# Performance work log

Hardware: AMD Instinct MI355X
Metric: run time of the kernel (lower is better)

The kernel has to match this reference:

```python
import jax, jax.numpy as jnp
import numpy as np

TOPK = 2  # n_activated
HID, INTER, E, SHARED_INTER = 2048, 1408, 14, 2816


def setup_inputs() -> dict:
    key = jax.random.key(0)
    ks = jax.random.split(key, 11)
    s = 0.02  # weight init scale
    return {
        "x": jax.random.normal(ks[0], (4, 512, HID), jnp.float32),
        "gate_w": jax.random.normal(ks[1], (E, HID), jnp.float32) * s,
        "cls_w": jax.random.normal(ks[2], (E, HID), jnp.float32) * s,
        "extra_scale": jax.random.normal(ks[3], (E,), jnp.float32) * 0.1,
        "extra_bias": jax.random.normal(ks[4], (E,), jnp.float32) * 0.01,
        "wg": jax.random.normal(ks[5], (E, INTER, HID), jnp.float32) * s,
        "wu": jax.random.normal(ks[6], (E, INTER, HID), jnp.float32) * s,
        "wd": jax.random.normal(ks[7], (E, HID, INTER), jnp.float32) * s,
        "sg": jax.random.normal(ks[8], (SHARED_INTER, HID), jnp.float32) * s,
        "su": jax.random.normal(ks[9], (SHARED_INTER, HID), jnp.float32) * s,
        "sd": jax.random.normal(ks[10], (HID, SHARED_INTER), jnp.float32) * s,
    }


def reference(x, gate_w, cls_w, extra_scale, extra_bias, wg, wu, wd, sg, su, sd):
    shape = x.shape
    d = shape[-1]
    xf = x.reshape(-1, d)                      # [T, d]
    T = xf.shape[0]
    n_exp = gate_w.shape[0]

    # Router: scores = softmax(|classifier(x) * silu(gate(x))|)
    logits = (xf @ cls_w.T) * jax.nn.silu(xf @ gate_w.T)        # [T, E]
    scores = jax.nn.softmax(jnp.abs(logits).astype(jnp.float32), axis=-1)
    biased = scores + extra_bias[None, :]
    _, idx = jax.lax.top_k(biased, TOPK)                         # [T, K]
    orig = 1.0 + scores * extra_scale[None, :]
    w = jnp.take_along_axis(orig, idx, axis=1).astype(x.dtype)   # [T, K]

    # Dense combine weights: zero for unrouted (token, expert) pairs.
    combine = jnp.zeros((T, n_exp), x.dtype).at[
        jnp.arange(T)[:, None], idx].add(w)                      # [T, E]

    # Routed experts (SwiGLU MLPs), computed densely then masked-combined.
    g = jax.nn.silu(jnp.einsum('td,efd->etf', xf, wg))           # [E, T, f]
    u = jnp.einsum('td,efd->etf', xf, wu)
    o = jnp.einsum('etf,edf->etd', g * u, wd)                    # [E, T, d]
    y = jnp.einsum('etd,te->td', o, combine)                     # [T, d]

    # Shared expert on all tokens.
    z = (jax.nn.silu(xf @ sg.T) * (xf @ su.T)) @ sd.T            # [T, d]

    return (y + z).reshape(shape)
```

## Files before the change

kernel.cpp:

```cpp
#include <hip/hip_runtime.h>

#define HID 2048
#define INTER 1408
#define NEXP 14
#define SINTER 2816
#define TTOK 2048
#define BM 384
#define BK 64

#define GLU_SH 264
#define GLU_RT 308
#define DWN_SH 96
#define DWN_RT 224

typedef short bf16x8 __attribute__((ext_vector_type(8)));
typedef float f32x4 __attribute__((ext_vector_type(4)));
typedef unsigned short u16x8 __attribute__((ext_vector_type(8)));

__device__ __forceinline__ unsigned short f2bf(float f) {
    __bf16 b = (__bf16)f;
    return __builtin_bit_cast(unsigned short, b);
}
__device__ __forceinline__ float bf2f(unsigned short u) {
    unsigned v = (unsigned)u << 16;
    return __builtin_bit_cast(float, v);
}
__device__ __forceinline__ unsigned swz(unsigned b) { return b ^ (((b >> 7) & 7u) << 4); }

__device__ __forceinline__ void gload16(const void* g, void* l) {
    __builtin_amdgcn_global_load_lds((__attribute__((address_space(1))) void*)g,
                                     (__attribute__((address_space(3))) void*)l, 16, 0, 0);
}
__device__ __forceinline__ void bsync() {
    __builtin_amdgcn_sched_barrier(0);
    __builtin_amdgcn_s_barrier();
    __builtin_amdgcn_sched_barrier(0);
}
#define WAIT_LGKM0 asm volatile("s_waitcnt lgkmcnt(0)" ::: "memory")

__global__ void k_zero(int* cnt) {
    if ((int)threadIdx.x < NEXP) cnt[threadIdx.x] = 0;
}

__global__ __launch_bounds__(256, 4) void k_router(
    const float* __restrict__ x,
    const float* __restrict__ gate_w, const float* __restrict__ cls_w,
    const float* __restrict__ escale, const float* __restrict__ ebias,
    int* __restrict__ cnt, int* __restrict__ etok, float* __restrict__ ew,
    unsigned short* __restrict__ xb) {
    const int lane = threadIdx.x & 63;
    const int tok = blockIdx.x * 4 + (threadIdx.x >> 6);
    const float* xr = x + (size_t)tok * HID + lane * 4;
    float4 xv[8];
#pragma unroll
    for (int i = 0; i < 8; i++) xv[i] = *(const float4*)(xr + i * 256);
    unsigned short* xbr = xb + (size_t)tok * HID + lane * 4;
#pragma unroll
    for (int i = 0; i < 8; i++) {
        ushort4 v;
        v.x = f2bf(xv[i].x); v.y = f2bf(xv[i].y);
        v.z = f2bf(xv[i].z); v.w = f2bf(xv[i].w);
        *(ushort4*)(xbr + i * 256) = v;
    }

    float sc[NEXP];
    float mx = 0.f;
#pragma unroll
    for (int e = 0; e < NEXP; e++) {
        const float* cw = cls_w + (size_t)e * HID + lane * 4;
        const float* gw = gate_w + (size_t)e * HID + lane * 4;
        float pc = 0.f, pg = 0.f;
        {
            float4 cv[8];
#pragma unroll
            for (int i = 0; i < 8; i++) cv[i] = *(const float4*)(cw + i * 256);
#pragma unroll
            for (int i = 0; i < 8; i++) {
                pc = fmaf(xv[i].x, cv[i].x, pc);
                pc = fmaf(xv[i].y, cv[i].y, pc);
                pc = fmaf(xv[i].z, cv[i].z, pc);
                pc = fmaf(xv[i].w, cv[i].w, pc);
            }
        }
        {
            float4 gv[8];
#pragma unroll
            for (int i = 0; i < 8; i++) gv[i] = *(const float4*)(gw + i * 256);
#pragma unroll
            for (int i = 0; i < 8; i++) {
                pg = fmaf(xv[i].x, gv[i].x, pg);
                pg = fmaf(xv[i].y, gv[i].y, pg);
                pg = fmaf(xv[i].z, gv[i].z, pg);
                pg = fmaf(xv[i].w, gv[i].w, pg);
            }
        }
#pragma unroll
        for (int o = 32; o >= 1; o >>= 1) {
            pc += __shfl_xor(pc, o);
            pg += __shfl_xor(pg, o);
        }
        float lg = pc * (pg / (1.f + __expf(-pg)));
        sc[e] = fabsf(lg);
        mx = fmaxf(mx, sc[e]);
    }
    float s = 0.f;
#pragma unroll
    for (int e = 0; e < NEXP; e++) { sc[e] = __expf(sc[e] - mx); s += sc[e]; }
    float inv = 1.f / s;
    int i1 = -1, i2 = -1;
    float b1 = -1e30f, b2 = -1e30f, v1 = 0.f, v2 = 0.f;
#pragma unroll
    for (int e = 0; e < NEXP; e++) {
        float sv = sc[e] * inv;
        float b = sv + ebias[e];
        if (b > b1) { b2 = b1; i2 = i1; v2 = v1; b1 = b; i1 = e; v1 = sv; }
        else if (b > b2) { b2 = b; i2 = e; v2 = sv; }
    }
    if (lane == 0) {
        float w1 = 1.f + v1 * escale[i1];
        float w2 = 1.f + v2 * escale[i2];
        int p1 = atomicAdd(&cnt[i1], 1);
        etok[i1 * TTOK + p1] = tok * 2;     ew[i1 * TTOK + p1] = w1;
        int p2 = atomicAdd(&cnt[i2], 1);
        etok[i2 * TTOK + p2] = tok * 2 + 1; ew[i2 * TTOK + p2] = w2;
    }
}

__global__ void k_offsets(const int* __restrict__ cnt, int* __restrict__ offs) {
    if (threadIdx.x == 0) {
        int a = 0;
        for (int e = 0; e < NEXP; e++) { offs[e] = a; a += cnt[e]; }
    }
}

__global__ __launch_bounds__(1024, 4) void k_glu16(
    const unsigned short* __restrict__ xb,
    const float* __restrict__ wg, const float* __restrict__ wu,
    const float* __restrict__ sg, const float* __restrict__ su,
    unsigned short* __restrict__ abuf, unsigned short* __restrict__ hbuf,
    const int* __restrict__ cnt, const int* __restrict__ offs,
    const int* __restrict__ etok) {
    __shared__ alignas(16) unsigned short sA[2][BM * BK];
    __shared__ alignas(16) unsigned short sBg[64 * BK];
    __shared__ alignas(16) unsigned short sBu[64 * BK];

    const int bx = blockIdx.x, t = threadIdx.x;
    const int lane = t & 63, w = t >> 6;
    const int wm = w >> 1, wn = w & 1;
    const int fr = lane & 15, fo = lane >> 4;

    const bool routed = bx >= GLU_SH;
    int n0, m_start, m_stop, obase, Ntot;
    const float *Bg, *Bu;
    unsigned short* outp;
    const int* etk = nullptr;
    if (routed) {
        int rx = bx - GLU_SH;
        int e = rx / 22; n0 = (rx % 22) * 64;
        int M = cnt[e];
        if (M <= 0) return;
        m_start = 0; m_stop = M; obase = offs[e]; Ntot = INTER;
        Bg = wg + ((size_t)e * INTER + n0) * HID;
        Bu = wu + ((size_t)e * INTER + n0) * HID;
        outp = abuf; etk = etok + e * TTOK;
    } else {
        n0 = (bx / 6) * 64;
        m_start = (bx % 6) * BM; m_stop = min(TTOK, m_start + BM);
        obase = 0; Ntot = SINTER;
        Bg = sg + (size_t)n0 * HID;
        Bu = su + (size_t)n0 * HID;
        outp = hbuf;
    }

    const int brow = t >> 4, bc4 = (t & 15) * 4;
    const float* srcG = Bg + (size_t)brow * HID + bc4;
    const float* srcU = Bu + (size_t)brow * HID + bc4;
    const unsigned wBo = swz((unsigned)(brow * 128 + bc4 * 2));

    unsigned aoff[3][2], boff[2][2];
#pragma unroll
    for (int mi = 0; mi < 3; mi++)
#pragma unroll
        for (int ks = 0; ks < 2; ks++)
            aoff[mi][ks] = swz((unsigned)((wm * 48 + mi * 16 + fr) * 128 + ks * 64 + fo * 16));
#pragma unroll
    for (int nj = 0; nj < 2; nj++)
#pragma unroll
        for (int ks = 0; ks < 2; ks++)
            boff[nj][ks] = swz((unsigned)((wn * 32 + nj * 16 + fr) * 128 + ks * 64 + fo * 16));

    const int arow_off = lane >> 3;
    const int achunk = (lane & 7) ^ arow_off;

    for (int m0 = m_start; m0 < m_stop; m0 += BM) {
        const int rv = min(m_stop - m0, BM);
        const unsigned short* srcA[3];
#pragma unroll
        for (int j = 0; j < 3; j++) {
            int r = (w * 3 + j) * 8 + arow_off;
            int rr = r < rv ? r : rv - 1;
            int tok = routed ? (etk[m0 + rr] >> 1) : (m0 + rr);
            srcA[j] = xb + (size_t)tok * HID + achunk * 8;
        }

        f32x4 ag[3][2], au[3][2];
#pragma unroll
        for (int mi = 0; mi < 3; mi++)
#pragma unroll
            for (int nj = 0; nj < 2; nj++) { ag[mi][nj] = {0.f,0.f,0.f,0.f}; au[mi][nj] = {0.f,0.f,0.f,0.f}; }

#pragma unroll
        for (int j = 0; j < 3; j++)
            gload16(srcA[j], (char*)sA + (w * 3 + j) * 1024);
        float4 gC = *(const float4*)(srcG);
        float4 uC = *(const float4*)(srcU);
        float4 gN, uN;

        for (int kk = 0; kk < HID / BK; ++kk) {
            const int cur = kk & 1;
            bsync();
            if (kk + 1 < HID / BK) {
                const int k0n = (kk + 1) * BK;
#pragma unroll
                for (int j = 0; j < 3; j++)
                    gload16(srcA[j] + k0n, (char*)sA + (cur ^ 1) * (BM * BK * 2) + (w * 3 + j) * 1024);
                gN = *(const float4*)(srcG + k0n);
                uN = *(const float4*)(srcU + k0n);
            }
            __builtin_amdgcn_sched_barrier(0);
            {
                ushort4 vg, vu;
                vg.x = f2bf(gC.x); vg.y = f2bf(gC.y); vg.z = f2bf(gC.z); vg.w = f2bf(gC.w);
                vu.x = f2bf(uC.x); vu.y = f2bf(uC.y); vu.z = f2bf(uC.z); vu.w = f2bf(uC.w);
                *(ushort4*)((char*)sBg + wBo) = vg;
                *(ushort4*)((char*)sBu + wBo) = vu;
            }
            WAIT_LGKM0;
            bsync();
            const char* sAc = (const char*)sA + cur * (BM * BK * 2);
#pragma unroll
            for (int ks = 0; ks < 2; ++ks) {
                bf16x8 af[3], gf[2], uf[2];
#pragma unroll
                for (int mi = 0; mi < 3; mi++) af[mi] = *(const bf16x8*)(sAc + aoff[mi][ks]);
#pragma unroll
                for (int nj = 0; nj < 2; nj++) {
                    gf[nj] = *(const bf16x8*)((const char*)sBg + boff[nj][ks]);
                    uf[nj] = *(const bf16x8*)((const char*)sBu + boff[nj][ks]);
                }
#pragma unroll
                for (int mi = 0; mi < 3; mi++)
#pragma unroll
                    for (int nj = 0; nj < 2; nj++) {
                        ag[mi][nj] = __builtin_amdgcn_mfma_f32_16x16x32_bf16(af[mi], gf[nj], ag[mi][nj], 0, 0, 0);
                        au[mi][nj] = __builtin_amdgcn_mfma_f32_16x16x32_bf16(af[mi], uf[nj], au[mi][nj], 0, 0, 0);
                    }
            }
            gC = gN; uC = uN;
        }

        char* sH = (char*)sA;
#pragma unroll
        for (int mi = 0; mi < 3; mi++)
#pragma unroll
            for (int jj = 0; jj < 4; jj++) {
                int r = wm * 48 + mi * 16 + fo * 4 + jj;
#pragma unroll
                for (int nj = 0; nj < 2; nj++) {
                    int c = wn * 32 + nj * 16 + fr;
                    float g = ag[mi][nj][jj];
                    float u = au[mi][nj][jj];
                    float h = (g / (1.f + __expf(-g))) * u;
                    *(unsigned short*)(sH + swz((unsigned)(r * 128 + c * 2))) = f2bf(h);
                }
            }
        WAIT_LGKM0;
        bsync();
#pragma unroll
        for (int q = 0; q < 3; q++) {
            int idx = q * 1024 + t;
            int r = idx >> 3, c = idx & 7;
            if (r < rv) {
                uint4 v = *(const uint4*)(sH + swz((unsigned)(r * 128 + c * 16)));
                *(uint4*)(outp + (size_t)(obase + m0 + r) * Ntot + n0 + c * 8) = v;
            }
        }
        bsync();
    }
}

__global__ __launch_bounds__(1024, 4) void k_down16(
    const unsigned short* __restrict__ abuf, const unsigned short* __restrict__ hbuf,
    const float* __restrict__ wd, const float* __restrict__ sd,
    unsigned short* __restrict__ slots,
    const int* __restrict__ cnt, const int* __restrict__ offs,
    const int* __restrict__ etok, const float* __restrict__ ew) {
    __shared__ alignas(16) unsigned short sA[2][BM * BK];
    __shared__ alignas(16) unsigned short sB[128 * BK];

    const int bx = blockIdx.x, t = threadIdx.x;
    const int lane = t & 63, w = t >> 6;
    const int wm = w >> 1, wn = w & 1;
    const int fr = lane & 15, fo = lane >> 4;

    const bool routed = bx >= DWN_SH;
    int n0, m_start, m_stop, K, KT;
    const float* W;
    const unsigned short* Abuf;
    size_t arow0 = 0;
    const int* etk = nullptr; const float* ewe = nullptr;
    if (routed) {
        int rx = bx - DWN_SH;
        int e = rx / 16; n0 = (rx % 16) * 128;
        int M = cnt[e];
        if (M <= 0) return;
        m_start = 0; m_stop = M;
        K = INTER; KT = INTER / BK;
        W = wd + (size_t)e * HID * INTER + (size_t)n0 * INTER;
        Abuf = abuf; arow0 = offs[e];
        etk = etok + e * TTOK; ewe = ew + e * TTOK;
    } else {
        n0 = (bx / 6) * 128;
        m_start = (bx % 6) * BM; m_stop = min(TTOK, m_start + BM);
        K = SINTER; KT = SINTER / BK;
        W = sd + (size_t)n0 * SINTER;
        Abuf = hbuf;
    }

    const int brow = t >> 3, bc8 = (t & 7) * 8;
    const float* srcB = W + (size_t)brow * K + bc8;
    const unsigned wBo = swz((unsigned)(brow * 128 + bc8 * 2));

    unsigned aoff[3][2], boff[4][2];
#pragma unroll
    for (int mi = 0; mi < 3; mi++)
#pragma unroll
        for (int ks = 0; ks < 2; ks++)
            aoff[mi][ks] = swz((unsigned)((wm * 48 + mi * 16 + fr) * 128 + ks * 64 + fo * 16));
#pragma unroll
    for (int nj = 0; nj < 4; nj++)
#pragma unroll
        for (int ks = 0; ks < 2; ks++)
            boff[nj][ks] = swz((unsigned)((wn * 64 + nj * 16 + fr) * 128 + ks * 64 + fo * 16));

    const int arow_off = lane >> 3;
    const int achunk = (lane & 7) ^ arow_off;

    for (int m0 = m_start; m0 < m_stop; m0 += BM) {
        const int rv = min(m_stop - m0, BM);
        const unsigned short* srcA[3];
#pragma unroll
        for (int j = 0; j < 3; j++) {
            int r = (w * 3 + j) * 8 + arow_off;
            int rr = r < rv ? r : rv - 1;
            srcA[j] = Abuf + (arow0 + m0 + rr) * (size_t)K + achunk * 8;
        }

        f32x4 ac[3][4];
#pragma unroll
        for (int mi = 0; mi < 3; mi++)
#pragma unroll
            for (int nj = 0; nj < 4; nj++) ac[mi][nj] = {0.f, 0.f, 0.f, 0.f};

#pragma unroll
        for (int j = 0; j < 3; j++)
            gload16(srcA[j], (char*)sA + (w * 3 + j) * 1024);
        float4 bC0 = *(const float4*)(srcB), bC1 = *(const float4*)(srcB + 4);
        float4 bN0, bN1;

        for (int kk = 0; kk < KT; ++kk) {
            const int cur = kk & 1;
            bsync();
            if (kk + 1 < KT) {
                const int k0n = (kk + 1) * BK;
#pragma unroll
                for (int j = 0; j < 3; j++)
                    gload16(srcA[j] + k0n, (char*)sA + (cur ^ 1) * (BM * BK * 2) + (w * 3 + j) * 1024);
                bN0 = *(const float4*)(srcB + k0n);
                bN1 = *(const float4*)(srcB + k0n + 4);
            }
            __builtin_amdgcn_sched_barrier(0);
            {
                bf16x8 v;
                v[0]=(short)f2bf(bC0.x); v[1]=(short)f2bf(bC0.y); v[2]=(short)f2bf(bC0.z); v[3]=(short)f2bf(bC0.w);
                v[4]=(short)f2bf(bC1.x); v[5]=(short)f2bf(bC1.y); v[6]=(short)f2bf(bC1.z); v[7]=(short)f2bf(bC1.w);
                *(bf16x8*)((char*)sB + wBo) = v;
            }
            WAIT_LGKM0;
            bsync();
            const char* sAc = (const char*)sA + cur * (BM * BK * 2);
#pragma unroll
            for (int ks = 0; ks < 2; ++ks) {
                bf16x8 af[3], bf[4];
#pragma unroll
                for (int mi = 0; mi < 3; mi++) af[mi] = *(const bf16x8*)(sAc + aoff[mi][ks]);
#pragma unroll
                for (int nj = 0; nj < 4; nj++) bf[nj] = *(const bf16x8*)((const char*)sB + boff[nj][ks]);
#pragma unroll
                for (int mi = 0; mi < 3; mi++)
#pragma unroll
                    for (int nj = 0; nj < 4; nj++)
                        ac[mi][nj] = __builtin_amdgcn_mfma_f32_16x16x32_bf16(af[mi], bf[nj], ac[mi][nj], 0, 0, 0);
            }
            bC0 = bN0; bC1 = bN1;
        }

        char* sH = (char*)sA;
#pragma unroll
        for (int p = 0; p < 2; p++) {
            if (wn == p) {
#pragma unroll
                for (int mi = 0; mi < 3; mi++)
#pragma unroll
                    for (int jj = 0; jj < 4; jj++) {
                        int r = wm * 48 + mi * 16 + fo * 4 + jj;
                        float wt = 1.f;
                        if (routed) wt = (r < rv) ? ewe[m0 + r] : 0.f;
#pragma unroll
                        for (int nj = 0; nj < 4; nj++) {
                            int c = nj * 16 + fr;
                            *(unsigned short*)(sH + swz((unsigned)(r * 128 + c * 2))) =
                                f2bf(ac[mi][nj][jj] * wt);
                        }
                    }
            }
            WAIT_LGKM0;
            bsync();
#pragma unroll
            for (int q = 0; q < 3; q++) {
                int idx = q * 1024 + t;
                int r = idx >> 3, c = idx & 7;
                if (r < rv) {
                    uint4 v = *(const uint4*)(sH + swz((unsigned)(r * 128 + c * 16)));
                    int tok, slice;
                    if (routed) { int entry = etk[m0 + r]; tok = entry >> 1; slice = entry & 1; }
                    else        { tok = m0 + r; slice = 2; }
                    *(uint4*)(slots + ((size_t)slice * TTOK + tok) * HID + n0 + p * 64 + c * 8) = v;
                }
            }
            bsync();
        }
    }
}

__global__ __launch_bounds__(256) void k_final(float* __restrict__ out,
                                               const unsigned short* __restrict__ slots) {
    size_t i = ((size_t)blockIdx.x * 256 + threadIdx.x) * 8;
    u16x8 s0 = *(const u16x8*)(slots + i);
    u16x8 s1 = *(const u16x8*)(slots + (size_t)TTOK * HID + i);
    u16x8 s2 = *(const u16x8*)(slots + (size_t)2 * TTOK * HID + i);
    float4 o0, o1;
    o0.x = bf2f(s0[0]) + bf2f(s1[0]) + bf2f(s2[0]);
    o0.y = bf2f(s0[1]) + bf2f(s1[1]) + bf2f(s2[1]);
    o0.z = bf2f(s0[2]) + bf2f(s1[2]) + bf2f(s2[2]);
    o0.w = bf2f(s0[3]) + bf2f(s1[3]) + bf2f(s2[3]);
    o1.x = bf2f(s0[4]) + bf2f(s1[4]) + bf2f(s2[4]);
    o1.y = bf2f(s0[5]) + bf2f(s1[5]) + bf2f(s2[5]);
    o1.z = bf2f(s0[6]) + bf2f(s1[6]) + bf2f(s2[6]);
    o1.w = bf2f(s0[7]) + bf2f(s1[7]) + bf2f(s2[7]);
    *(float4*)(out + i) = o0;
    *(float4*)(out + i + 4) = o1;
}

extern "C" void kernel_launch(void* const* d_in, const int* in_sizes, int n_in,
                              void* d_out, int out_size, void* d_ws, size_t ws_size,
                              hipStream_t stream) {
    const float* x = (const float*)d_in[0];
    const float* gate_w = (const float*)d_in[1];
    const float* cls_w = (const float*)d_in[2];
    const float* escale = (const float*)d_in[3];
    const float* ebias = (const float*)d_in[4];
    const float* wg = (const float*)d_in[5];
    const float* wu = (const float*)d_in[6];
    const float* wd = (const float*)d_in[7];
    const float* sg = (const float*)d_in[8];
    const float* su = (const float*)d_in[9];
    const float* sd = (const float*)d_in[10];
    float* out = (float*)d_out;

    char* ws = (char*)d_ws;
    size_t o = 0;
    auto alloc = [&](size_t bytes) {
        char* p = ws + o;
        o += (bytes + 255) & ~(size_t)255;
        return p;
    };
    unsigned short* xb    = (unsigned short*)alloc((size_t)TTOK * HID * 2);
    unsigned short* hbuf  = (unsigned short*)alloc((size_t)TTOK * SINTER * 2);
    unsigned short* abuf  = (unsigned short*)alloc((size_t)2 * TTOK * INTER * 2);
    unsigned short* slots = (unsigned short*)alloc((size_t)3 * TTOK * HID * 2);
    int* cnt              = (int*)alloc(256);
    int* offs             = (int*)alloc(256);
    int* etok             = (int*)alloc((size_t)NEXP * TTOK * 4);
    float* ew             = (float*)alloc((size_t)NEXP * TTOK * 4);

    k_zero<<<1, 64, 0, stream>>>(cnt);
    k_router<<<512, 256, 0, stream>>>(x, gate_w, cls_w, escale, ebias, cnt, etok, ew, xb);
    k_offsets<<<1, 64, 0, stream>>>(cnt, offs);
    k_glu16<<<GLU_SH + GLU_RT, 1024, 0, stream>>>(
        xb, wg, wu, sg, su, abuf, hbuf, cnt, offs, etok);
    k_down16<<<DWN_SH + DWN_RT, 1024, 0, stream>>>(
        abuf, hbuf, wd, sd, slots, cnt, offs, etok, ew);
    k_final<<<2048, 256, 0, stream>>>(out, slots);
}
```

Before: 537.4 us.

## Retile GLU and down GEMMs to 256x128 and 256x256 blocks

Changes the GLU kernel from 384x64 to 256x128 output tiles and the down kernel from 384x128 to 256x256 tiles. Warp layouts, LDS buffers, swizzles and epilogue indexing change to match, and routed blocks are now placed first in the grid. Larger N tiles mean each A tile is reused across more output columns and fewer blocks reload the same activations, which is meant to cut redundant global traffic and the per-block fp32-to-bf16 weight conversion. The cost is fewer blocks (330 and 176) on a large GPU, which may lower occupancy and worsen load balance across uneven expert counts, and more accumulator registers per thread in the down kernel.

```diff
diff --git a/kernel.cpp b/kernel.cpp
--- a/kernel.cpp
+++ b/kernel.cpp
@@ -5,13 +5,12 @@
 #define NEXP 14
 #define SINTER 2816
 #define TTOK 2048
-#define BM 384
 #define BK 64
 
-#define GLU_SH 264
-#define GLU_RT 308
-#define DWN_SH 96
-#define DWN_RT 224
+#define GLU_RT 154
+#define GLU_SH 176
+#define DWN_SH 64
+#define DWN_RT 112
 
 typedef short bf16x8 __attribute__((ext_vector_type(8)));
 typedef float f32x4 __attribute__((ext_vector_type(4)));
@@ -25,7 +24,8 @@
     unsigned v = (unsigned)u << 16;
     return __builtin_bit_cast(float, v);
 }
-__device__ __forceinline__ unsigned swz(unsigned b) { return b ^ (((b >> 7) & 7u) << 4); }
+__device__ __forceinline__ unsigned swz(unsigned b)    { return b ^ (((b >> 7) & 7u) << 4); }
+__device__ __forceinline__ unsigned swz256(unsigned b) { return b ^ (((b >> 8) & 7u) << 4); }
 
 __device__ __forceinline__ void gload16(const void* g, void* l) {
     __builtin_amdgcn_global_load_lds((__attribute__((address_space(1))) void*)g,
@@ -37,6 +37,7 @@
     __builtin_amdgcn_sched_barrier(0);
 }
 #define WAIT_LGKM0 asm volatile("s_waitcnt lgkmcnt(0)" ::: "memory")
+#define MFMA16(a, b, c) __builtin_amdgcn_mfma_f32_16x16x32_bf16(a, b, c, 0, 0, 0)
 
 __global__ void k_zero(int* cnt) {
     if ((int)threadIdx.x < NEXP) cnt[threadIdx.x] = 0;
@@ -133,30 +134,29 @@
     }
 }
 
-__global__ __launch_bounds__(1024, 4) void k_glu16(
+__global__ __launch_bounds__(1024, 4) void k_glu17(
     const unsigned short* __restrict__ xb,
     const float* __restrict__ wg, const float* __restrict__ wu,
     const float* __restrict__ sg, const float* __restrict__ su,
     unsigned short* __restrict__ abuf, unsigned short* __restrict__ hbuf,
     const int* __restrict__ cnt, const int* __restrict__ offs,
     const int* __restrict__ etok) {
-    __shared__ alignas(16) unsigned short sA[2][BM * BK];
-    __shared__ alignas(16) unsigned short sBg[64 * BK];
-    __shared__ alignas(16) unsigned short sBu[64 * BK];
+    __shared__ alignas(16) unsigned short sA[2][256 * BK];
+    __shared__ alignas(16) unsigned short sBg[128 * BK];
+    __shared__ alignas(16) unsigned short sBu[128 * BK];
 
     const int bx = blockIdx.x, t = threadIdx.x;
     const int lane = t & 63, w = t >> 6;
     const int wm = w >> 1, wn = w & 1;
     const int fr = lane & 15, fo = lane >> 4;
 
-    const bool routed = bx >= GLU_SH;
+    const bool routed = bx < GLU_RT;
     int n0, m_start, m_stop, obase, Ntot;
     const float *Bg, *Bu;
     unsigned short* outp;
     const int* etk = nullptr;
     if (routed) {
-        int rx = bx - GLU_SH;
-        int e = rx / 22; n0 = (rx % 22) * 64;
+        int e = bx / 11; n0 = (bx % 11) * 128;
         int M = cnt[e];
         if (M <= 0) return;
         m_start = 0; m_stop = M; obase = offs[e]; Ntot = INTER;
@@ -164,57 +164,58 @@
         Bu = wu + ((size_t)e * INTER + n0) * HID;
         outp = abuf; etk = etok + e * TTOK;
     } else {
-        n0 = (bx / 6) * 64;
-        m_start = (bx % 6) * BM; m_stop = min(TTOK, m_start + BM);
+        int sx = bx - GLU_RT;
+        n0 = (sx >> 3) * 128;
+        m_start = (sx & 7) * 256; m_stop = m_start + 256;
         obase = 0; Ntot = SINTER;
         Bg = sg + (size_t)n0 * HID;
         Bu = su + (size_t)n0 * HID;
         outp = hbuf;
     }
 
-    const int brow = t >> 4, bc4 = (t & 15) * 4;
-    const float* srcG = Bg + (size_t)brow * HID + bc4;
-    const float* srcU = Bu + (size_t)brow * HID + bc4;
-    const unsigned wBo = swz((unsigned)(brow * 128 + bc4 * 2));
-
-    unsigned aoff[3][2], boff[2][2];
-#pragma unroll
-    for (int mi = 0; mi < 3; mi++)
+    const int brow = t >> 3, bc8 = (t & 7) * 8;
+    const float* srcG = Bg + (size_t)brow * HID + bc8;
+    const float* srcU = Bu + (size_t)brow * HID + bc8;
+    const unsigned wBo = swz((unsigned)(brow * 128 + bc8 * 2));
+
+    unsigned aoff[2][2], boff[4][2];
+#pragma unroll
+    for (int mi = 0; mi < 2; mi++)
 #pragma unroll
         for (int ks = 0; ks < 2; ks++)
-            aoff[mi][ks] = swz((unsigned)((wm * 48 + mi * 16 + fr) * 128 + ks * 64 + fo * 16));
-#pragma unroll
-    for (int nj = 0; nj < 2; nj++)
+            aoff[mi][ks] = swz((unsigned)((wm * 32 + mi * 16 + fr) * 128 + ks * 64 + fo * 16));
+#pragma unroll
+    for (int nj = 0; nj < 4; nj++)
 #pragma unroll
         for (int ks = 0; ks < 2; ks++)
-            boff[nj][ks] = swz((unsigned)((wn * 32 + nj * 16 + fr) * 128 + ks * 64 + fo * 16));
+            boff[nj][ks] = swz((unsigned)((wn * 64 + nj * 16 + fr) * 128 + ks * 64 + fo * 16));
 
     const int arow_off = lane >> 3;
     const int achunk = (lane & 7) ^ arow_off;
 
-    for (int m0 = m_start; m0 < m_stop; m0 += BM) {
-        const int rv = min(m_stop - m0, BM);
-        const unsigned short* srcA[3];
-#pragma unroll
-        for (int j = 0; j < 3; j++) {
-            int r = (w * 3 + j) * 8 + arow_off;
+    for (int m0 = m_start; m0 < m_stop; m0 += 256) {
+        const int rv = min(m_stop - m0, 256);
+        const unsigned short* srcA[2];
+#pragma unroll
+        for (int j = 0; j < 2; j++) {
+            int r = w * 16 + j * 8 + arow_off;
             int rr = r < rv ? r : rv - 1;
             int tok = routed ? (etk[m0 + rr] >> 1) : (m0 + rr);
             srcA[j] = xb + (size_t)tok * HID + achunk * 8;
         }
 
-        f32x4 ag[3][2], au[3][2];
-#pragma unroll
-        for (int mi = 0; mi < 3; mi++)
-#pragma unroll
-            for (int nj = 0; nj < 2; nj++) { ag[mi][nj] = {0.f,0.f,0.f,0.f}; au[mi][nj] = {0.f,0.f,0.f,0.f}; }
-
-#pragma unroll
-        for (int j = 0; j < 3; j++)
-            gload16(srcA[j], (char*)sA + (w * 3 + j) * 1024);
-        float4 gC = *(const float4*)(srcG);
-        float4 uC = *(const float4*)(srcU);
-        float4 gN, uN;
+        f32x4 ag[2][4], au[2][4];
+#pragma unroll
+        for (int mi = 0; mi < 2; mi++)
+#pragma unroll
+            for (int nj = 0; nj < 4; nj++) { ag[mi][nj] = {0.f,0.f,0.f,0.f}; au[mi][nj] = {0.f,0.f,0.f,0.f}; }
+
+#pragma unroll
+        for (int j = 0; j < 2; j++)
+            gload16(srcA[j], (char*)sA + w * 2048 + j * 1024);
+        float4 gC0 = *(const float4*)(srcG),     gC1 = *(const float4*)(srcG + 4);
+        float4 uC0 = *(const float4*)(srcU),     uC1 = *(const float4*)(srcU + 4);
+        float4 gN0, gN1, uN0, uN1;
 
         for (int kk = 0; kk < HID / BK; ++kk) {
             const int cur = kk & 1;
@@ -222,85 +223,88 @@
             if (kk + 1 < HID / BK) {
                 const int k0n = (kk + 1) * BK;
 #pragma unroll
-                for (int j = 0; j < 3; j++)
-                    gload16(srcA[j] + k0n, (char*)sA + (cur ^ 1) * (BM * BK * 2) + (w * 3 + j) * 1024);
-                gN = *(const float4*)(srcG + k0n);
-                uN = *(const float4*)(srcU + k0n);
+                for (int j = 0; j < 2; j++)
+                    gload16(srcA[j] + k0n, (char*)sA + (cur ^ 1) * 32768 + w * 2048 + j * 1024);
+                gN0 = *(const float4*)(srcG + k0n); gN1 = *(const float4*)(srcG + k0n + 4);
+                uN0 = *(const float4*)(srcU + k0n); uN1 = *(const float4*)(srcU + k0n + 4);
             }
             __builtin_amdgcn_sched_barrier(0);
             {
-                ushort4 vg, vu;
-                vg.x = f2bf(gC.x); vg.y = f2bf(gC.y); vg.z = f2bf(gC.z); vg.w = f2bf(gC.w);
-                vu.x = f2bf(uC.x); vu.y = f2bf(uC.y); vu.z = f2bf(uC.z); vu.w = f2bf(uC.w);
-                *(ushort4*)((char*)sBg + wBo) = vg;
-                *(ushort4*)((char*)sBu + wBo) = vu;
+                bf16x8 vg, vu;
+                vg[0]=(short)f2bf(gC0.x); vg[1]=(short)f2bf(gC0.y); vg[2]=(short)f2bf(gC0.z); vg[3]=(short)f2bf(gC0.w);
+                vg[4]=(short)f2bf(gC1.x); vg[5]=(short)f2bf(gC1.y); vg[6]=(short)f2bf(gC1.z); vg[7]=(short)f2bf(gC1.w);
+                vu[0]=(short)f2bf(uC0.x); vu[1]=(short)f2bf(uC0.y); vu[2]=(short)f2bf(uC0.z); vu[3]=(short)f2bf(uC0.w);
+                vu[4]=(short)f2bf(uC1.x); vu[5]=(short)f2bf(uC1.y); vu[6]=(short)f2bf(uC1.z); vu[7]=(short)f2bf(uC1.w);
+                *(bf16x8*)((char*)sBg + wBo) = vg;
+                *(bf16x8*)((char*)sBu + wBo) = vu;
             }
             WAIT_LGKM0;
             bsync();
-            const char* sAc = (const char*)sA + cur * (BM * BK * 2);
+            const char* sAc = (const char*)sA + cur * 32768;
 #pragma unroll
             for (int ks = 0; ks < 2; ++ks) {
-                bf16x8 af[3], gf[2], uf[2];
-#pragma unroll
-                for (int mi = 0; mi < 3; mi++) af[mi] = *(const bf16x8*)(sAc + aoff[mi][ks]);
-#pragma unroll
-                for (int nj = 0; nj < 2; nj++) {
+                bf16x8 af[2], gf[4], uf[4];
+#pragma unroll
+                for (int mi = 0; mi < 2; mi++) af[mi] = *(const bf16x8*)(sAc + aoff[mi][ks]);
+#pragma unroll
+                for (int nj = 0; nj < 4; nj++) {
                     gf[nj] = *(const bf16x8*)((const char*)sBg + boff[nj][ks]);
                     uf[nj] = *(const bf16x8*)((const char*)sBu + boff[nj][ks]);
                 }
 #pragma unroll
-                for (int mi = 0; mi < 3; mi++)
-#pragma unroll
-                    for (int nj = 0; nj < 2; nj++) {
-                        ag[mi][nj] = __builtin_amdgcn_mfma_f32_16x16x32_bf16(af[mi], gf[nj], ag[mi][nj], 0, 0, 0);
-                        au[mi][nj] = __builtin_amdgcn_mfma_f32_16x16x32_bf16(af[mi], uf[nj], au[mi][nj], 0, 0, 0);
+                for (int mi = 0; mi < 2; mi++)
+#pragma unroll
+                    for (int nj = 0; nj < 4; nj++) {
+                        ag[mi][nj] = MFMA16(af[mi], gf[nj], ag[mi][nj]);
+                        au[mi][nj] = MFMA16(af[mi], uf[nj], au[mi][nj]);
                     }
             }
-            gC = gN; uC = uN;
-        }
-
+            gC0 = gN0; gC1 = gN1; uC0 = uN0; uC1 = uN1;
+        }
+
+        bsync();
         char* sH = (char*)sA;
 #pragma unroll
-        for (int mi = 0; mi < 3; mi++)
+        for (int mi = 0; mi < 2; mi++)
 #pragma unroll
             for (int jj = 0; jj < 4; jj++) {
-                int r = wm * 48 + mi * 16 + fo * 4 + jj;
-#pragma unroll
-                for (int nj = 0; nj < 2; nj++) {
-                    int c = wn * 32 + nj * 16 + fr;
+                int r = wm * 32 + mi * 16 + fo * 4 + jj;
+#pragma unroll
+                for (int nj = 0; nj < 4; nj++) {
+                    int c = wn * 64 + nj * 16 + fr;
                     float g = ag[mi][nj][jj];
                     float u = au[mi][nj][jj];
                     float h = (g / (1.f + __expf(-g))) * u;
-                    *(unsigned short*)(sH + swz((unsigned)(r * 128 + c * 2))) = f2bf(h);
+                    *(unsigned short*)(sH + swz256((unsigned)(r * 256 + c * 2))) = f2bf(h);
                 }
             }
         WAIT_LGKM0;
         bsync();
 #pragma unroll
-        for (int q = 0; q < 3; q++) {
+        for (int q = 0; q < 4; q++) {
             int idx = q * 1024 + t;
-            int r = idx >> 3, c = idx & 7;
+            int r = idx >> 4, c16 = idx & 15;
             if (r < rv) {
-                uint4 v = *(const uint4*)(sH + swz((unsigned)(r * 128 + c * 16)));
-                *(uint4*)(outp + (size_t)(obase + m0 + r) * Ntot + n0 + c * 8) = v;
+                uint4 v = *(const uint4*)(sH + swz256((unsigned)(r * 256 + c16 * 16)));
+                *(uint4*)(outp + (size_t)(obase + m0 + r) * Ntot + n0 + c16 * 8) = v;
             }
         }
         bsync();
     }
 }
 
-__global__ __launch_bounds__(1024, 4) void k_down16(
+__global__ __launch_bounds__(1024, 4) void k_down17(
     const unsigned short* __restrict__ abuf, const unsigned short* __restrict__ hbuf,
     const float* __restrict__ wd, const float* __restrict__ sd,
     unsigned short* __restrict__ slots,
     const int* __restrict__ cnt, const int* __restrict__ offs,
     const int* __restrict__ etok, const float* __restrict__ ew) {
-    __shared__ alignas(16) unsigned short sA[2][BM * BK];
-    __shared__ alignas(16) unsigned short sB[128 * BK];
+    __shared__ alignas(16) unsigned short sA[2][256 * BK];
+    __shared__ alignas(16) unsigned short sB[256 * BK];
 
     const int bx = blockIdx.x, t = threadIdx.x;
     const int lane = t & 63, w = t >> 6;
-    const int wm = w >> 1, wn = w & 1;
+    const int wm = w >> 2, wn = w & 3;
     const int fr = lane & 15, fo = lane >> 4;
 
     const bool routed = bx >= DWN_SH;
@@ -311,7 +315,7 @@
     const int* etk = nullptr; const float* ewe = nullptr;
     if (routed) {
         int rx = bx - DWN_SH;
-        int e = rx / 16; n0 = (rx % 16) * 128;
+        int e = rx >> 3; n0 = (rx & 7) * 256;
         int M = cnt[e];
         if (M <= 0) return;
         m_start = 0; m_stop = M;
@@ -320,23 +324,24 @@
         Abuf = abuf; arow0 = offs[e];
         etk = etok + e * TTOK; ewe = ew + e * TTOK;
     } else {
-        n0 = (bx / 6) * 128;
-        m_start = (bx % 6) * BM; m_stop = min(TTOK, m_start + BM);
+        n0 = (bx >> 3) * 256;
+        m_start = (bx & 7) * 256; m_stop = m_start + 256;
         K = SINTER; KT = SINTER / BK;
         W = sd + (size_t)n0 * SINTER;
         Abuf = hbuf;
     }
 
-    const int brow = t >> 3, bc8 = (t & 7) * 8;
-    const float* srcB = W + (size_t)brow * K + bc8;
-    const unsigned wBo = swz((unsigned)(brow * 128 + bc8 * 2));
-
-    unsigned aoff[3][2], boff[4][2];
-#pragma unroll
-    for (int mi = 0; mi < 3; mi++)
+    const int brow = t >> 2, bc16 = (t & 3) * 16;
+    const float* srcB = W + (size_t)brow * K + bc16;
+    const unsigned wBo0 = swz((unsigned)(brow * 128 + bc16 * 2));
+    const unsigned wBo1 = swz((unsigned)(brow * 128 + bc16 * 2 + 16));
+
+    unsigned aoff[4][2], boff[4][2];
+#pragma unroll
+    for (int mi = 0; mi < 4; mi++)
 #pragma unroll
         for (int ks = 0; ks < 2; ks++)
-            aoff[mi][ks] = swz((unsigned)((wm * 48 + mi * 16 + fr) * 128 + ks * 64 + fo * 16));
+            aoff[mi][ks] = swz((unsigned)((wm * 64 + mi * 16 + fr) * 128 + ks * 64 + fo * 16));
 #pragma unroll
     for (int nj = 0; nj < 4; nj++)
 #pragma unroll
@@ -346,27 +351,28 @@
     const int arow_off = lane >> 3;
     const int achunk = (lane & 7) ^ arow_off;
 
-    for (int m0 = m_start; m0 < m_stop; m0 += BM) {
-        const int rv = min(m_stop - m0, BM);
-        const unsigned short* srcA[3];
-#pragma unroll
-        for (int j = 0; j < 3; j++) {
-            int r = (w * 3 + j) * 8 + arow_off;
+    for (int m0 = m_start; m0 < m_stop; m0 += 256) {
+        const int rv = min(m_stop - m0, 256);
+        const unsigned short* srcA[2];
+#pragma unroll
+        for (int j = 0; j < 2; j++) {
+            int r = w * 16 + j * 8 + arow_off;
             int rr = r < rv ? r : rv - 1;
             srcA[j] = Abuf + (arow0 + m0 + rr) * (size_t)K + achunk * 8;
         }
 
-        f32x4 ac[3][4];
-#pragma unroll
-        for (int mi = 0; mi < 3; mi++)
+        f32x4 ac[4][4];
+#pragma unroll
+        for (int mi = 0; mi < 4; mi++)
 #pragma unroll
             for (int nj = 0; nj < 4; nj++) ac[mi][nj] = {0.f, 0.f, 0.f, 0.f};
 
 #pragma unroll
-        for (int j = 0; j < 3; j++)
-            gload16(srcA[j], (char*)sA + (w * 3 + j) * 1024);
-        float4 bC0 = *(const float4*)(srcB), bC1 = *(const float4*)(srcB + 4);
-        float4 bN0, bN1;
+        for (int j = 0; j < 2; j++)
+            gload16(srcA[j], (char*)sA + w * 2048 + j * 1024);
+        float4 bC0 = *(const float4*)(srcB),      bC1 = *(const float4*)(srcB + 4);
+        float4 bC2 = *(const float4*)(srcB + 8),  bC3 = *(const float4*)(srcB + 12);
+        float4 bN0, bN1, bN2, bN3;
 
         for (int kk = 0; kk < KT; ++kk) {
             const int cur = kk & 1;
@@ -374,52 +380,56 @@
             if (kk + 1 < KT) {
                 const int k0n = (kk + 1) * BK;
 #pragma unroll
-                for (int j = 0; j < 3; j++)
-                    gload16(srcA[j] + k0n, (char*)sA + (cur ^ 1) * (BM * BK * 2) + (w * 3 + j) * 1024);
-                bN0 = *(const float4*)(srcB + k0n);
-                bN1 = *(const float4*)(srcB + k0n + 4);
+                for (int j = 0; j < 2; j++)
+                    gload16(srcA[j] + k0n, (char*)sA + (cur ^ 1) * 32768 + w * 2048 + j * 1024);
+                bN0 = *(const float4*)(srcB + k0n);      bN1 = *(const float4*)(srcB + k0n + 4);
+                bN2 = *(const float4*)(srcB + k0n + 8);  bN3 = *(const float4*)(srcB + k0n + 12);
             }
             __builtin_amdgcn_sched_barrier(0);
             {
-                bf16x8 v;
-                v[0]=(short)f2bf(bC0.x); v[1]=(short)f2bf(bC0.y); v[2]=(short)f2bf(bC0.z); v[3]=(short)f2bf(bC0.w);
-                v[4]=(short)f2bf(bC1.x); v[5]=(short)f2bf(bC1.y); v[6]=(short)f2bf(bC1.z); v[7]=(short)f2bf(bC1.w);
-                *(bf16x8*)((char*)sB + wBo) = v;
+                bf16x8 v0, v1;
+                v0[0]=(short)f2bf(bC0.x); v0[1]=(short)f2bf(bC0.y); v0[2]=(short)f2bf(bC0.z); v0[3]=(short)f2bf(bC0.w);
+                v0[4]=(short)f2bf(bC1.x); v0[5]=(short)f2bf(bC1.y); v0[6]=(short)f2bf(bC1.z); v0[7]=(short)f2bf(bC1.w);
+                v1[0]=(short)f2bf(bC2.x); v1[1]=(short)f2bf(bC2.y); v1[2]=(short)f2bf(bC2.z); v1[3]=(short)f2bf(bC2.w);
+                v1[4]=(short)f2bf(bC3.x); v1[5]=(short)f2bf(bC3.y); v1[6]=(short)f2bf(bC3.z); v1[7]=(short)f2bf(bC3.w);
+                *(bf16x8*)((char*)sB + wBo0) = v0;
+                *(bf16x8*)((char*)sB + wBo1) = v1;
             }
             WAIT_LGKM0;
             bsync();
-            const char* sAc = (const char*)sA + cur * (BM * BK * 2);
+            const char* sAc = (const char*)sA + cur * 32768;
 #pragma unroll
             for (int ks = 0; ks < 2; ++ks) {
-                bf16x8 af[3], bf[4];
-#pragma unroll
-                for (int mi = 0; mi < 3; mi++) af[mi] = *(const bf16x8*)(sAc + aoff[mi][ks]);
+                bf16x8 af[4], bf[4];
+#pragma unroll
+                for (int mi = 0; mi < 4; mi++) af[mi] = *(const bf16x8*)(sAc + aoff[mi][ks]);
 #pragma unroll
                 for (int nj = 0; nj < 4; nj++) bf[nj] = *(const bf16x8*)((const char*)sB + boff[nj][ks]);
 #pragma unroll
-                for (int mi = 0; mi < 3; mi++)
+                for (int mi = 0; mi < 4; mi++)
 #pragma unroll
                     for (int nj = 0; nj < 4; nj++)
-                        ac[mi][nj] = __builtin_amdgcn_mfma_f32_16x16x32_bf16(af[mi], bf[nj], ac[mi][nj], 0, 0, 0);
-            }
-            bC0 = bN0; bC1 = bN1;
-        }
-
+                        ac[mi][nj] = MFMA16(af[mi], bf[nj], ac[mi][nj]);
+            }
+            bC0 = bN0; bC1 = bN1; bC2 = bN2; bC3 = bN3;
+        }
+
+        bsync();
         char* sH = (char*)sA;
 #pragma unroll
         for (int p = 0; p < 2; p++) {
-            if (wn == p) {
-#pragma unroll
-                for (int mi = 0; mi < 3; mi++)
+            if ((wn >> 1) == p) {
+#pragma unroll
+                for (int mi = 0; mi < 4; mi++)
 #pragma unroll
                     for (int jj = 0; jj < 4; jj++) {
-                        int r = wm * 48 + mi * 16 + fo * 4 + jj;
+                        int r = wm * 64 + mi * 16 + fo * 4 + jj;
                         float wt = 1.f;
                         if (routed) wt = (r < rv) ? ewe[m0 + r] : 0.f;
 #pragma unroll
                         for (int nj = 0; nj < 4; nj++) {
-                            int c = nj * 16 + fr;
-                            *(unsigned short*)(sH + swz((unsigned)(r * 128 + c * 2))) =
+                            int c = (wn & 1) * 64 + nj * 16 + fr;
+                            *(unsigned short*)(sH + swz256((unsigned)(r * 256 + c * 2))) =
                                 f2bf(ac[mi][nj][jj] * wt);
                         }
                     }
@@ -427,15 +437,15 @@
             WAIT_LGKM0;
             bsync();
 #pragma unroll
-            for (int q = 0; q < 3; q++) {
+            for (int q = 0; q < 4; q++) {
                 int idx = q * 1024 + t;
-                int r = idx >> 3, c = idx & 7;
+                int r = idx >> 4, c16 = idx & 15;
                 if (r < rv) {
-                    uint4 v = *(const uint4*)(sH + swz((unsigned)(r * 128 + c * 16)));
+                    uint4 v = *(const uint4*)(sH + swz256((unsigned)(r * 256 + c16 * 16)));
                     int tok, slice;
                     if (routed) { int entry = etk[m0 + r]; tok = entry >> 1; slice = entry & 1; }
                     else        { tok = m0 + r; slice = 2; }
-                    *(uint4*)(slots + ((size_t)slice * TTOK + tok) * HID + n0 + p * 64 + c * 8) = v;
+                    *(uint4*)(slots + ((size_t)slice * TTOK + tok) * HID + n0 + p * 128 + c16 * 8) = v;
                 }
             }
             bsync();
@@ -497,9 +507,9 @@
     k_zero<<<1, 64, 0, stream>>>(cnt);
     k_router<<<512, 256, 0, stream>>>(x, gate_w, cls_w, escale, ebias, cnt, etok, ew, xb);
     k_offsets<<<1, 64, 0, stream>>>(cnt, offs);
-    k_glu16<<<GLU_SH + GLU_RT, 1024, 0, stream>>>(
+    k_glu17<<<GLU_RT + GLU_SH, 1024, 0, stream>>>(
         xb, wg, wu, sg, su, abuf, hbuf, cnt, offs, etok);
-    k_down16<<<DWN_SH + DWN_RT, 1024, 0, stream>>>(
+    k_down17<<<DWN_SH + DWN_RT, 1024, 0, stream>>>(
         abuf, hbuf, wd, sd, slots, cnt, offs, etok, ew);
     k_final<<<2048, 256, 0, stream>>>(out, slots);
 }
```

Result: slower. 1.024 ms (+90.6%).
